# Performance work log

Measured on AMD Instinct MI355X. Metric: run time of the kernel, lower is better.

Reference implementation:

```python
import jax, jax.numpy as jnp
import numpy as np
import math

D_MODEL = 1152
D_K = 1152
NUM_HEADS = 8
HEAD_DIM = D_K // NUM_HEADS  # 144
SIGMA = 2.0
EPS = 1e-6


def rope_2d(keys, positions):
    # keys: [B, N, D]; positions: [B, N, 2] float (x, y)
    B, N, D = keys.shape
    half = D // 2
    quarter = D // 4
    idx = jnp.arange(quarter, dtype=keys.dtype)
    theta = 1.0 / (10000.0 ** (2.0 * idx / half))  # [quarter]
    fx = positions[..., 0][..., None] * theta  # [B, N, quarter]
    fy = positions[..., 1][..., None] * theta

    def apply_rope(part, f):
        p = part.reshape(B, N, quarter, 2)
        c, s = jnp.cos(f), jnp.sin(f)
        o1 = p[..., 0] * c - p[..., 1] * s
        o2 = p[..., 0] * s + p[..., 1] * c
        return jnp.stack([o1, o2], axis=-1).reshape(B, N, half)

    return jnp.concatenate(
        [apply_rope(keys[..., :half], fx), apply_rope(keys[..., half:], fy)], axis=-1
    )


def layernorm_nobias(x, w, eps=EPS):
    mu = jnp.mean(x, axis=-1, keepdims=True)
    var = jnp.mean(jnp.square(x - mu), axis=-1, keepdims=True)
    return (x - mu) * jax.lax.rsqrt(var + eps) * w


def setup_inputs() -> dict:
    key = jax.random.key(0)
    ks = jax.random.split(key, 9)
    T, HW, M = 64, 729, 512
    features = jax.random.normal(ks[0], (T, HW, D_MODEL), dtype=jnp.float32)
    tracks = jax.random.uniform(ks[1], (T, M, 2), dtype=jnp.float32) * 27.0
    track_tokens = jax.random.normal(ks[2], (T, M, D_MODEL), dtype=jnp.float32)
    feature_positions = jax.random.uniform(ks[3], (HW, 2), dtype=jnp.float32) * 27.0
    sc = 1.0 / math.sqrt(D_MODEL)
    # weights stored [in, out]; torch Linear computes x @ W.T with W [out, in]
    W_q = jax.random.normal(ks[4], (D_MODEL, D_K), dtype=jnp.float32) * sc
    W_k = jax.random.normal(ks[5], (D_MODEL, D_K), dtype=jnp.float32) * sc
    q_norm_w = jnp.ones((D_K,), dtype=jnp.float32)
    k_norm_w = jnp.ones((D_K,), dtype=jnp.float32)
    out_proj_w = jax.random.normal(ks[6], (D_MODEL, D_MODEL), dtype=jnp.float32) * sc
    return {
        "features": features,
        "tracks": tracks,
        "track_tokens": track_tokens,
        "feature_positions": feature_positions,
        "W_q": W_q,
        "W_k": W_k,
        "q_norm_w": q_norm_w,
        "k_norm_w": k_norm_w,
        "out_proj_w": out_proj_w,
    }


def reference(features, tracks, track_tokens, feature_positions,
              W_q, W_k, q_norm_w, k_norm_w, out_proj_w):
    T, HW, _ = features.shape
    M = tracks.shape[1]
    Q = track_tokens @ W_q  # [T, M, d_k]
    K = features @ W_k      # [T, HW, d_k]
    feat_pos = jnp.broadcast_to(feature_positions[None], (T, HW, 2))
    K = rope_2d(K, feat_pos)
    Q = layernorm_nobias(Q, q_norm_w)
    K = layernorm_nobias(K, k_norm_w)
    Qh = Q.reshape(T, M, NUM_HEADS, HEAD_DIM).transpose(0, 2, 1, 3)   # [T,H,M,dh]
    Kh = K.reshape(T, HW, NUM_HEADS, HEAD_DIM).transpose(0, 2, 1, 3)  # [T,H,HW,dh]
    Vh = features.reshape(T, HW, NUM_HEADS, -1).transpose(0, 2, 1, 3) # [T,H,HW,dv]
    scores = jnp.einsum("thmd,thnd->thmn", Qh, Kh) / math.sqrt(HEAD_DIM)
    # Gaussian spatial bias: -||track - feat||^2 / (2 sigma^2), shared across heads
    diff = tracks[:, :, None, :] - feature_positions[None, None, :, :]  # [T,M,HW,2]
    dist2 = jnp.sum(jnp.square(diff), axis=-1)  # [T,M,HW]
    bias = -dist2 / (2.0 * SIGMA ** 2)
    scores = scores + bias[:, None, :, :]
    attn = jax.nn.softmax(scores, axis=-1)
    sampled = jnp.einsum("thmn,thnd->thmd", attn, Vh)  # [T,H,M,dv]
    sampled = sampled.transpose(0, 2, 1, 3).reshape(T, M, -1)
    return sampled @ out_proj_w
```

## Files before the change

### kernel.cpp

```cpp
#include <hip/hip_runtime.h>
#include <hip/hip_bf16.h>
#include <math.h>

typedef float f32x4 __attribute__((ext_vector_type(4)));
typedef __bf16 bf16x8 __attribute__((ext_vector_type(8)));

#define T_N 64
#define HW_N 729
#define M_N 512
#define DM 1152
#define NH 8
#define DH 144
#define MQ 32768
#define MK 46656
#define MK_PAD 46720

#define SZ_FEAT ((size_t)MK_PAD * DM * 2)
#define SZ_Q    ((size_t)MQ * DM * 2)
#define SZ_W    ((size_t)DM * DM * 2)
#define OFF_FEAT ((size_t)0)
#define OFF_KN   (OFF_FEAT + SZ_FEAT)
#define OFF_AQ   (OFF_KN + SZ_FEAT)
#define OFF_QN   (OFF_AQ + SZ_Q)
#define OFF_WT   (OFF_QN + SZ_Q)
#define WS_NEED  (OFF_WT + 3 * SZ_W)

__global__ __launch_bounds__(256) void cvt_bf16(const float* __restrict__ src,
                                                __bf16* __restrict__ dst,
                                                long valid4, long total4) {
    long i = (long)blockIdx.x * 256 + threadIdx.x;
    if (i >= total4) return;
    float4 f = {0.f, 0.f, 0.f, 0.f};
    if (i < valid4) f = ((const float4*)src)[i];
    __bf16 tmp[4] = {(__bf16)f.x, (__bf16)f.y, (__bf16)f.z, (__bf16)f.w};
    *((uint2*)(dst + i * 4)) = *((uint2*)tmp);
}

__global__ __launch_bounds__(256) void transpose_w(const float* __restrict__ W,
                                                   __bf16* __restrict__ Wt) {
    __shared__ float tile[32][33];
    const int k0 = blockIdx.x * 32, n0 = blockIdx.y * 32;
    const int tx = threadIdx.x, ty = threadIdx.y;
    #pragma unroll
    for (int i = 0; i < 32; i += 8)
        tile[ty + i][tx] = W[(long)(k0 + ty + i) * DM + n0 + tx];
    __syncthreads();
    #pragma unroll
    for (int i = 0; i < 32; i += 8)
        Wt[(long)(n0 + ty + i) * DM + k0 + tx] = (__bf16)tile[tx][ty + i];
}

template<bool STORE_BF16>
__global__ __launch_bounds__(256) void gemm_bt(const __bf16* __restrict__ A,
                                               const __bf16* __restrict__ Bt,
                                               void* __restrict__ Cout) {
    __shared__ __align__(16) __bf16 As[128 * 40];
    __shared__ __align__(16) __bf16 Bs[128 * 40];
    const int tid  = threadIdx.x;
    const int wave = tid >> 6, lane = tid & 63;
    const int quad = lane >> 4, l16 = lane & 15;
    const int wr = wave >> 1, wc = wave & 1;
    const long m0 = (long)blockIdx.x * 128;
    const long n0 = (long)blockIdx.y * 128;
    f32x4 acc[4][4] = {};
    for (int kt = 0; kt < 36; ++kt) {
        const int k0 = kt * 32;
        __syncthreads();
        #pragma unroll
        for (int s = 0; s < 2; ++s) {
            const int c = s * 256 + tid;
            const int row = c >> 2, kc = c & 3;
            uint4 va = *(const uint4*)(A  + (m0 + row) * DM + k0 + kc * 8);
            uint4 vb = *(const uint4*)(Bt + (n0 + row) * DM + k0 + kc * 8);
            *(uint4*)(As + row * 40 + kc * 8) = va;
            *(uint4*)(Bs + row * 40 + kc * 8) = vb;
        }
        __syncthreads();
        bf16x8 af[4], bfr[4];
        #pragma unroll
        for (int i = 0; i < 4; ++i)
            af[i] = *(const bf16x8*)(As + (wr * 64 + i * 16 + l16) * 40 + quad * 8);
        #pragma unroll
        for (int j = 0; j < 4; ++j)
            bfr[j] = *(const bf16x8*)(Bs + (wc * 64 + j * 16 + l16) * 40 + quad * 8);
        #pragma unroll
        for (int i = 0; i < 4; ++i)
            #pragma unroll
            for (int j = 0; j < 4; ++j)
                acc[i][j] = __builtin_amdgcn_mfma_f32_16x16x32_bf16(af[i], bfr[j], acc[i][j], 0, 0, 0);
    }
    #pragma unroll
    for (int i = 0; i < 4; ++i) {
        #pragma unroll
        for (int j = 0; j < 4; ++j) {
            #pragma unroll
            for (int r = 0; r < 4; ++r) {
                const long row = m0 + wr * 64 + i * 16 + quad * 4 + r;
                const long col = n0 + wc * 64 + j * 16 + l16;
                if constexpr (STORE_BF16)
                    ((__bf16*)Cout)[row * DM + col] = (__bf16)acc[i][j][r];
                else
                    ((float*)Cout)[row * DM + col] = acc[i][j][r];
            }
        }
    }
}

__global__ __launch_bounds__(256) void ln_q(__bf16* __restrict__ Q, const float* __restrict__ w) {
    const long row = blockIdx.x;
    __bf16* p = Q + row * DM;
    const int tid = threadIdx.x;
    float v[5];
    int nv = 0;
    float s = 0.f, s2 = 0.f;
    for (int i = tid; i < DM; i += 256) {
        float x = (float)p[i];
        v[nv++] = x; s += x; s2 += x * x;
    }
    #pragma unroll
    for (int o = 32; o > 0; o >>= 1) { s += __shfl_down(s, o); s2 += __shfl_down(s2, o); }
    __shared__ float red[8];
    if ((tid & 63) == 0) { red[tid >> 6] = s; red[4 + (tid >> 6)] = s2; }
    __syncthreads();
    const float S  = red[0] + red[1] + red[2] + red[3];
    const float S2 = red[4] + red[5] + red[6] + red[7];
    const float mu  = S * (1.f / DM);
    const float var = S2 * (1.f / DM) - mu * mu;
    const float rstd = rsqrtf(var + 1e-6f);
    nv = 0;
    for (int i = tid; i < DM; i += 256)
        p[i] = (__bf16)((v[nv++] - mu) * rstd * w[i]);
}

__global__ __launch_bounds__(256) void rope_ln_k(__bf16* __restrict__ K,
                                                 const float* __restrict__ fpos,
                                                 const float* __restrict__ w) {
    const long row = blockIdx.x;
    const int hw = (int)(row % HW_N);
    const float px = fpos[hw * 2 + 0];
    const float py = fpos[hw * 2 + 1];
    __bf16* p = K + row * DM;
    __shared__ float buf[DM];
    __shared__ float red[8];
    const int tid = threadIdx.x;
    float s = 0.f, s2 = 0.f;
    for (int pr = tid; pr < 576; pr += 256) {
        const bool isx = pr < 288;
        const int  i   = isx ? pr : pr - 288;
        const int  off = isx ? 2 * i : 576 + 2 * i;
        const float pos = isx ? px : py;
        const float theta = powf(10000.f, -(float)i * (1.f / 288.f));
        float sn, cs;
        sincosf(pos * theta, &sn, &cs);
        const float a = (float)p[off], b = (float)p[off + 1];
        const float o1 = a * cs - b * sn;
        const float o2 = a * sn + b * cs;
        buf[off] = o1; buf[off + 1] = o2;
        s += o1 + o2; s2 += o1 * o1 + o2 * o2;
    }
    #pragma unroll
    for (int o = 32; o > 0; o >>= 1) { s += __shfl_down(s, o); s2 += __shfl_down(s2, o); }
    if ((tid & 63) == 0) { red[tid >> 6] = s; red[4 + (tid >> 6)] = s2; }
    __syncthreads();
    const float S  = red[0] + red[1] + red[2] + red[3];
    const float S2 = red[4] + red[5] + red[6] + red[7];
    const float mu  = S * (1.f / DM);
    const float var = S2 * (1.f / DM) - mu * mu;
    const float rstd = rsqrtf(var + 1e-6f);
    for (int i = tid; i < DM; i += 256)
        p[i] = (__bf16)((buf[i] - mu) * rstd * w[i]);
}

__global__ __launch_bounds__(256) void attn(const __bf16* __restrict__ Qn,
                                            const __bf16* __restrict__ Kn,
                                            const __bf16* __restrict__ Vf,
                                            const float* __restrict__ tracks,
                                            const float* __restrict__ fpos,
                                            __bf16* __restrict__ Out) {
    const int b  = blockIdx.x;
    const int qt = b & 7;
    const int th = b >> 3;
    const int h  = th & 7;
    const int t  = th >> 3;
    __shared__ __align__(16) __bf16 Qs[64 * 168];
    __shared__ __align__(16) __bf16 Ks[32 * 168];
    __shared__ __align__(16) __bf16 Vs[32 * 168];
    __shared__ __align__(16) __bf16 Ps[64 * 40];
    __shared__ float trkx[64], trky[64], fpx[32], fpy[32];
    const int tid = threadIdx.x;
    const int wave = tid >> 6, lane = tid & 63;
    const int quad = lane >> 4, l16 = lane & 15;

    {
        const __bf16* qb = Qn + ((long)t * M_N + qt * 64) * DM + h * DH;
        for (int c = tid; c < 64 * 20; c += 256) {
            const int r = c / 20, cc = c % 20;
            uint4 v = {0u, 0u, 0u, 0u};
            if (cc < 18) v = *(const uint4*)(qb + (long)r * DM + cc * 8);
            *(uint4*)(Qs + r * 168 + cc * 8) = v;
        }
        if (tid < 64) {
            const long qr = (long)t * M_N + qt * 64 + tid;
            trkx[tid] = tracks[qr * 2 + 0];
            trky[tid] = tracks[qr * 2 + 1];
        }
    }

    float mrow[4], lrow[4];
    #pragma unroll
    for (int r = 0; r < 4; ++r) { mrow[r] = -1e30f; lrow[r] = 0.f; }
    f32x4 Ot[9] = {};

    for (int kt = 0; kt < 23; ++kt) {
        const int kv0 = kt * 32;
        __syncthreads();
        {
            const __bf16* kb = Kn + ((long)t * HW_N + kv0) * DM + h * DH;
            const __bf16* vb = Vf + ((long)t * HW_N + kv0) * DM + h * DH;
            for (int c = tid; c < 32 * 20; c += 256) {
                const int r = c / 20, cc = c % 20;
                uint4 vk = {0u,0u,0u,0u}, vv = {0u,0u,0u,0u};
                if (cc < 18) {
                    vk = *(const uint4*)(kb + (long)r * DM + cc * 8);
                    vv = *(const uint4*)(vb + (long)r * DM + cc * 8);
                }
                *(uint4*)(Ks + r * 168 + cc * 8) = vk;
                *(uint4*)(Vs + r * 168 + cc * 8) = vv;
            }
            if (tid < 32) {
                const int hw = kv0 + tid;
                if (hw < HW_N) { fpx[tid] = fpos[hw * 2]; fpy[tid] = fpos[hw * 2 + 1]; }
                else           { fpx[tid] = 0.f;          fpy[tid] = 0.f; }
            }
        }
        __syncthreads();
        f32x4 sc[2] = {};
        #pragma unroll
        for (int kc = 0; kc < 5; ++kc) {
            const bf16x8 aq = *(const bf16x8*)(Qs + (wave * 16 + l16) * 168 + kc * 32 + quad * 8);
            #pragma unroll
            for (int j = 0; j < 2; ++j) {
                const bf16x8 bk = *(const bf16x8*)(Ks + (j * 16 + l16) * 168 + kc * 32 + quad * 8);
                sc[j] = __builtin_amdgcn_mfma_f32_16x16x32_bf16(aq, bk, sc[j], 0, 0, 0);
            }
        }
        float fx[2], fy[2]; bool msk[2];
        #pragma unroll
        for (int j = 0; j < 2; ++j) {
            const int cl = j * 16 + l16;
            fx[j] = fpx[cl]; fy[j] = fpy[cl];
            msk[j] = (kv0 + cl) >= HW_N;
        }
        float pvals[4][2];
        float alpha[4];
        #pragma unroll
        for (int r = 0; r < 4; ++r) {
            const int brow = wave * 16 + quad * 4 + r;
            const float tx = trkx[brow], ty = trky[brow];
            float mx = -1e30f;
            #pragma unroll
            for (int j = 0; j < 2; ++j) {
                const float dx = tx - fx[j], dy = ty - fy[j];
                float sv = sc[j][r] * (1.f / 12.f) - (dx * dx + dy * dy) * 0.125f;
                if (msk[j]) sv = -1e30f;
                pvals[r][j] = sv;
                mx = fmaxf(mx, sv);
            }
            #pragma unroll
            for (int o = 1; o < 16; o <<= 1) mx = fmaxf(mx, __shfl_xor(mx, o));
            const float mn = fmaxf(mrow[r], mx);
            alpha[r] = __expf(mrow[r] - mn);
            float rs = 0.f;
            #pragma unroll
            for (int j = 0; j < 2; ++j) {
                const float pv = __expf(pvals[r][j] - mn);
                pvals[r][j] = pv; rs += pv;
            }
            #pragma unroll
            for (int o = 1; o < 16; o <<= 1) rs += __shfl_xor(rs, o);
            lrow[r] = lrow[r] * alpha[r] + rs;
            mrow[r] = mn;
        }
        #pragma unroll
        for (int d = 0; d < 9; ++d)
            #pragma unroll
            for (int r = 0; r < 4; ++r)
                Ot[d][r] *= alpha[r];
        #pragma unroll
        for (int r = 0; r < 4; ++r)
            #pragma unroll
            for (int j = 0; j < 2; ++j)
                Ps[(wave * 16 + quad * 4 + r) * 40 + j * 16 + l16] = (__bf16)pvals[r][j];
        __syncthreads();
        const bf16x8 ap = *(const bf16x8*)(Ps + (wave * 16 + l16) * 40 + quad * 8);
        #pragma unroll
        for (int d = 0; d < 9; ++d) {
            bf16x8 bv;
            #pragma unroll
            for (int jj = 0; jj < 8; ++jj)
                bv[jj] = Vs[(quad * 8 + jj) * 168 + d * 16 + l16];
            Ot[d] = __builtin_amdgcn_mfma_f32_16x16x32_bf16(ap, bv, Ot[d], 0, 0, 0);
        }
    }
    #pragma unroll
    for (int d = 0; d < 9; ++d) {
        #pragma unroll
        for (int r = 0; r < 4; ++r) {
            const long row = (long)t * M_N + qt * 64 + wave * 16 + quad * 4 + r;
            Out[row * DM + h * DH + d * 16 + l16] = (__bf16)(Ot[d][r] / lrow[r]);
        }
    }
}

extern "C" void kernel_launch(void* const* d_in, const int* in_sizes, int n_in,
                              void* d_out, int out_size, void* d_ws, size_t ws_size,
                              hipStream_t stream) {
    const float* features   = (const float*)d_in[0];
    const float* tracks     = (const float*)d_in[1];
    const float* tok        = (const float*)d_in[2];
    const float* fpos       = (const float*)d_in[3];
    const float* W_q        = (const float*)d_in[4];
    const float* W_k        = (const float*)d_in[5];
    const float* q_w        = (const float*)d_in[6];
    const float* k_w        = (const float*)d_in[7];
    const float* W_o        = (const float*)d_in[8];

    if (ws_size < WS_NEED) return;

    char* ws = (char*)d_ws;
    __bf16* feat_bf = (__bf16*)(ws + OFF_FEAT);
    __bf16* kn      = (__bf16*)(ws + OFF_KN);
    __bf16* tok_bf  = (__bf16*)(ws + OFF_AQ);
    __bf16* qn      = (__bf16*)(ws + OFF_QN);
    __bf16* wt_q    = (__bf16*)(ws + OFF_WT);
    __bf16* wt_k    = (__bf16*)(ws + OFF_WT + SZ_W);
    __bf16* wt_o    = (__bf16*)(ws + OFF_WT + 2 * SZ_W);

    {
        const long valid4 = (long)MK * DM / 4, total4 = (long)MK_PAD * DM / 4;
        cvt_bf16<<<(int)((total4 + 255) / 256), 256, 0, stream>>>(features, feat_bf, valid4, total4);
    }
    {
        const long n4 = (long)MQ * DM / 4;
        cvt_bf16<<<(int)((n4 + 255) / 256), 256, 0, stream>>>(tok, tok_bf, n4, n4);
    }
    dim3 tb(32, 8);
    transpose_w<<<dim3(36, 36), tb, 0, stream>>>(W_q, wt_q);
    transpose_w<<<dim3(36, 36), tb, 0, stream>>>(W_k, wt_k);
    transpose_w<<<dim3(36, 36), tb, 0, stream>>>(W_o, wt_o);

    gemm_bt<true><<<dim3(MQ / 128, DM / 128), 256, 0, stream>>>(tok_bf, wt_q, qn);
    gemm_bt<true><<<dim3(MK_PAD / 128, DM / 128), 256, 0, stream>>>(feat_bf, wt_k, kn);

    ln_q<<<MQ, 256, 0, stream>>>(qn, q_w);
    rope_ln_k<<<MK, 256, 0, stream>>>(kn, fpos, k_w);

    __bf16* sampled = tok_bf;
    attn<<<T_N * NH * (M_N / 64), 256, 0, stream>>>(qn, kn, feat_bf, tracks, fpos, sampled);

    gemm_bt<false><<<dim3(MQ / 128, DM / 128), 256, 0, stream>>>(sampled, wt_o, d_out);
}
```

Before: 1.819 ms.

## Rework attention tiling with pre-transposed V and async LDS loads in GEMM

Attention now handles 128 queries per block with 64-key tiles, reads Q and K fragments directly from global memory instead of staging them in LDS, and loads V from a new pre-transposed bf16 layout so the PV MFMA operands become contiguous vector loads rather than scalar gathers. The GEMM switches to global_load_lds async copies with an XOR-swizzled unpadded LDS layout to avoid bank conflicts. A new transpose_v kernel costs an extra pass over features, and the workspace is reorganised so feat_bf and vt share one region. The rope theta is computed with exp2f instead of powf.

New measurement: 1.739 ms. 4.4% less time.

```diff
diff --git a/kernel.cpp b/kernel.cpp
--- a/kernel.cpp
+++ b/kernel.cpp
@@ -7,6 +7,7 @@
 
 #define T_N 64
 #define HW_N 729
+#define HW_P 736
 #define M_N 512
 #define DM 1152
 #define NH 8
@@ -16,14 +17,22 @@
 #define MK_PAD 46720
 
 #define SZ_FEAT ((size_t)MK_PAD * DM * 2)
+#define SZ_VT   ((size_t)T_N * NH * DH * HW_P * 2)
+#define SZ_OV   (SZ_VT > SZ_FEAT ? SZ_VT : SZ_FEAT)
 #define SZ_Q    ((size_t)MQ * DM * 2)
 #define SZ_W    ((size_t)DM * DM * 2)
-#define OFF_FEAT ((size_t)0)
-#define OFF_KN   (OFF_FEAT + SZ_FEAT)
-#define OFF_AQ   (OFF_KN + SZ_FEAT)
-#define OFF_QN   (OFF_AQ + SZ_Q)
-#define OFF_WT   (OFF_QN + SZ_Q)
+#define OFF_KN   ((size_t)0)
+#define OFF_TOK  (OFF_KN + SZ_FEAT)
+#define OFF_QN   (OFF_TOK + SZ_Q)
+#define OFF_OV   (OFF_QN + SZ_Q)
+#define OFF_WT   (OFF_OV + SZ_OV)
 #define WS_NEED  (OFF_WT + 3 * SZ_W)
+
+__device__ __forceinline__ void async_copy16(void* lds, const void* g) {
+    __builtin_amdgcn_global_load_lds(
+        (const __attribute__((address_space(1))) void*)g,
+        (__attribute__((address_space(3))) void*)lds, 16, 0, 0);
+}
 
 __global__ __launch_bounds__(256) void cvt_bf16(const float* __restrict__ src,
                                                 __bf16* __restrict__ dst,
@@ -50,18 +59,42 @@
         Wt[(long)(n0 + ty + i) * DM + k0 + tx] = (__bf16)tile[tx][ty + i];
 }
 
+__global__ __launch_bounds__(256) void transpose_v(const float* __restrict__ f,
+                                                   __bf16* __restrict__ vt) {
+    __shared__ float tile[32][149];
+    const int hw0 = blockIdx.x * 32, h = blockIdx.y, t = blockIdx.z;
+    const int tid = threadIdx.x;
+    for (int c = tid; c < 32 * 36; c += 256) {
+        const int r = c / 36, s = c % 36;
+        const int hw = hw0 + r;
+        float4 v = {0.f, 0.f, 0.f, 0.f};
+        if (hw < HW_N) v = *(const float4*)(f + ((long)t * HW_N + hw) * DM + h * DH + s * 4);
+        tile[r][s * 4 + 0] = v.x; tile[r][s * 4 + 1] = v.y;
+        tile[r][s * 4 + 2] = v.z; tile[r][s * 4 + 3] = v.w;
+    }
+    __syncthreads();
+    for (int c = tid; c < DH * 4; c += 256) {
+        const int d = c >> 2, s = c & 3;
+        __bf16 tmp[8];
+        #pragma unroll
+        for (int i = 0; i < 8; ++i) tmp[i] = (__bf16)tile[s * 8 + i][d];
+        *(uint4*)(vt + ((long)(t * NH + h) * DH + d) * HW_P + hw0 + s * 8) = *(uint4*)tmp;
+    }
+}
+
 template<bool STORE_BF16>
 __global__ __launch_bounds__(256) void gemm_bt(const __bf16* __restrict__ A,
                                                const __bf16* __restrict__ Bt,
                                                void* __restrict__ Cout) {
-    __shared__ __align__(16) __bf16 As[128 * 40];
-    __shared__ __align__(16) __bf16 Bs[128 * 40];
+    __shared__ __align__(16) __bf16 As[128 * 32];
+    __shared__ __align__(16) __bf16 Bs[128 * 32];
     const int tid  = threadIdx.x;
     const int wave = tid >> 6, lane = tid & 63;
     const int quad = lane >> 4, l16 = lane & 15;
     const int wr = wave >> 1, wc = wave & 1;
     const long m0 = (long)blockIdx.x * 128;
     const long n0 = (long)blockIdx.y * 128;
+    const int swzr = quad ^ ((l16 >> 1) & 3);
     f32x4 acc[4][4] = {};
     for (int kt = 0; kt < 36; ++kt) {
         const int k0 = kt * 32;
@@ -69,20 +102,19 @@
         #pragma unroll
         for (int s = 0; s < 2; ++s) {
             const int c = s * 256 + tid;
-            const int row = c >> 2, kc = c & 3;
-            uint4 va = *(const uint4*)(A  + (m0 + row) * DM + k0 + kc * 8);
-            uint4 vb = *(const uint4*)(Bt + (n0 + row) * DM + k0 + kc * 8);
-            *(uint4*)(As + row * 40 + kc * 8) = va;
-            *(uint4*)(Bs + row * 40 + kc * 8) = vb;
+            const int row = c >> 2;
+            const int gkc = (c & 3) ^ ((c >> 3) & 3);
+            async_copy16(As + c * 8, A  + (m0 + row) * DM + k0 + gkc * 8);
+            async_copy16(Bs + c * 8, Bt + (n0 + row) * DM + k0 + gkc * 8);
         }
         __syncthreads();
         bf16x8 af[4], bfr[4];
         #pragma unroll
         for (int i = 0; i < 4; ++i)
-            af[i] = *(const bf16x8*)(As + (wr * 64 + i * 16 + l16) * 40 + quad * 8);
+            af[i] = *(const bf16x8*)(As + (wr * 64 + i * 16 + l16) * 32 + swzr * 8);
         #pragma unroll
         for (int j = 0; j < 4; ++j)
-            bfr[j] = *(const bf16x8*)(Bs + (wc * 64 + j * 16 + l16) * 40 + quad * 8);
+            bfr[j] = *(const bf16x8*)(Bs + (wc * 64 + j * 16 + l16) * 32 + swzr * 8);
         #pragma unroll
         for (int i = 0; i < 4; ++i)
             #pragma unroll
@@ -149,7 +181,7 @@
         const int  i   = isx ? pr : pr - 288;
         const int  off = isx ? 2 * i : 576 + 2 * i;
         const float pos = isx ? px : py;
-        const float theta = powf(10000.f, -(float)i * (1.f / 288.f));
+        const float theta = exp2f((float)i * -0.046137890206768924f);
         float sn, cs;
         sincosf(pos * theta, &sn, &cs);
         const float a = (float)p[off], b = (float)p[off + 1];
@@ -171,143 +203,144 @@
         p[i] = (__bf16)((buf[i] - mu) * rstd * w[i]);
 }
 
-__global__ __launch_bounds__(256) void attn(const __bf16* __restrict__ Qn,
-                                            const __bf16* __restrict__ Kn,
-                                            const __bf16* __restrict__ Vf,
-                                            const float* __restrict__ tracks,
-                                            const float* __restrict__ fpos,
-                                            __bf16* __restrict__ Out) {
+__global__ __launch_bounds__(256, 3) void attn(const __bf16* __restrict__ Qn,
+                                               const __bf16* __restrict__ Kn,
+                                               const __bf16* __restrict__ Vt,
+                                               const float* __restrict__ tracks,
+                                               const float* __restrict__ fpos,
+                                               __bf16* __restrict__ Out) {
+    __shared__ __align__(16) __bf16 VtL[DH * 72];
+    __shared__ __align__(16) __bf16 Ps[128 * 72];
+    __shared__ float2 trkL[128];
     const int b  = blockIdx.x;
-    const int qt = b & 7;
-    const int th = b >> 3;
+    const int qt = b & 3;
+    const int th = b >> 2;
     const int h  = th & 7;
     const int t  = th >> 3;
-    __shared__ __align__(16) __bf16 Qs[64 * 168];
-    __shared__ __align__(16) __bf16 Ks[32 * 168];
-    __shared__ __align__(16) __bf16 Vs[32 * 168];
-    __shared__ __align__(16) __bf16 Ps[64 * 40];
-    __shared__ float trkx[64], trky[64], fpx[32], fpy[32];
     const int tid = threadIdx.x;
     const int wave = tid >> 6, lane = tid & 63;
     const int quad = lane >> 4, l16 = lane & 15;
-
-    {
-        const __bf16* qb = Qn + ((long)t * M_N + qt * 64) * DM + h * DH;
-        for (int c = tid; c < 64 * 20; c += 256) {
-            const int r = c / 20, cc = c % 20;
-            uint4 v = {0u, 0u, 0u, 0u};
-            if (cc < 18) v = *(const uint4*)(qb + (long)r * DM + cc * 8);
-            *(uint4*)(Qs + r * 168 + cc * 8) = v;
-        }
-        if (tid < 64) {
-            const long qr = (long)t * M_N + qt * 64 + tid;
-            trkx[tid] = tracks[qr * 2 + 0];
-            trky[tid] = tracks[qr * 2 + 1];
-        }
-    }
-
-    float mrow[4], lrow[4];
-    #pragma unroll
-    for (int r = 0; r < 4; ++r) { mrow[r] = -1e30f; lrow[r] = 0.f; }
-    f32x4 Ot[9] = {};
-
-    for (int kt = 0; kt < 23; ++kt) {
-        const int kv0 = kt * 32;
-        __syncthreads();
-        {
-            const __bf16* kb = Kn + ((long)t * HW_N + kv0) * DM + h * DH;
-            const __bf16* vb = Vf + ((long)t * HW_N + kv0) * DM + h * DH;
-            for (int c = tid; c < 32 * 20; c += 256) {
-                const int r = c / 20, cc = c % 20;
-                uint4 vk = {0u,0u,0u,0u}, vv = {0u,0u,0u,0u};
-                if (cc < 18) {
-                    vk = *(const uint4*)(kb + (long)r * DM + cc * 8);
-                    vv = *(const uint4*)(vb + (long)r * DM + cc * 8);
+    const int wq = wave * 32;
+
+    if (tid < 128) trkL[tid] = ((const float2*)tracks)[(long)t * M_N + qt * 128 + tid];
+
+    const __bf16* qb = Qn + ((long)t * M_N + qt * 128 + wq) * DM + h * DH;
+    const __bf16* kb = Kn + (long)t * HW_N * DM + h * DH;
+    const __bf16* vb = Vt + (long)(t * NH + h) * DH * HW_P;
+    const __bf16* zpg = Kn + (size_t)MK * DM;
+
+    f32x4 Ot[2][9] = {};
+    float mrow[2][4], lrow[2][4];
+    #pragma unroll
+    for (int rt = 0; rt < 2; ++rt)
+        #pragma unroll
+        for (int r = 0; r < 4; ++r) { mrow[rt][r] = -1e30f; lrow[rt][r] = 0.f; }
+
+    for (int kt = 0; kt < 12; ++kt) {
+        const int kv0 = kt * 64;
+        __syncthreads();
+        for (int c = tid; c < DH * 9; c += 256) {
+            const int r = c / 9, s = c % 9;
+            const __bf16* g = (s < 8 && (kv0 + s * 8 + 8) <= HW_P)
+                                ? vb + (long)r * HW_P + kv0 + s * 8 : zpg;
+            async_copy16(VtL + c * 8, g);
+        }
+        __syncthreads();
+        f32x4 sc[2][4] = {};
+        #pragma unroll
+        for (int kc = 0; kc < 5; ++kc) {
+            bf16x8 aq[2];
+            #pragma unroll
+            for (int rt = 0; rt < 2; ++rt) {
+                uint4 u = {0u, 0u, 0u, 0u};
+                if (kc < 4 || quad < 2)
+                    u = *(const uint4*)(qb + (long)(rt * 16 + l16) * DM + kc * 32 + quad * 8);
+                aq[rt] = *(bf16x8*)&u;
+            }
+            #pragma unroll
+            for (int jt = 0; jt < 4; ++jt) {
+                const bf16x8 bk = *(const bf16x8*)(kb + (long)(kv0 + jt * 16 + l16) * DM + kc * 32 + quad * 8);
+                #pragma unroll
+                for (int rt = 0; rt < 2; ++rt)
+                    sc[rt][jt] = __builtin_amdgcn_mfma_f32_16x16x32_bf16(aq[rt], bk, sc[rt][jt], 0, 0, 0);
+            }
+        }
+        float fx[4], fy[4]; bool msk[4];
+        #pragma unroll
+        for (int jt = 0; jt < 4; ++jt) {
+            const int kv = kv0 + jt * 16 + l16;
+            msk[jt] = kv >= HW_N;
+            float2 fp = {0.f, 0.f};
+            if (!msk[jt]) fp = ((const float2*)fpos)[kv];
+            fx[jt] = fp.x; fy[jt] = fp.y;
+        }
+        float alpha[2][4];
+        #pragma unroll
+        for (int rt = 0; rt < 2; ++rt) {
+            #pragma unroll
+            for (int r = 0; r < 4; ++r) {
+                const int row = wq + rt * 16 + quad * 4 + r;
+                const float tx = trkL[row].x, ty = trkL[row].y;
+                float sv[4];
+                float mx = -1e30f;
+                #pragma unroll
+                for (int jt = 0; jt < 4; ++jt) {
+                    const float dx = tx - fx[jt], dy = ty - fy[jt];
+                    float v = sc[rt][jt][r] * (1.f / 12.f) - (dx * dx + dy * dy) * 0.125f;
+                    if (msk[jt]) v = -1e30f;
+                    sv[jt] = v;
+                    mx = fmaxf(mx, v);
                 }
-                *(uint4*)(Ks + r * 168 + cc * 8) = vk;
-                *(uint4*)(Vs + r * 168 + cc * 8) = vv;
-            }
-            if (tid < 32) {
-                const int hw = kv0 + tid;
-                if (hw < HW_N) { fpx[tid] = fpos[hw * 2]; fpy[tid] = fpos[hw * 2 + 1]; }
-                else           { fpx[tid] = 0.f;          fpy[tid] = 0.f; }
-            }
-        }
-        __syncthreads();
-        f32x4 sc[2] = {};
-        #pragma unroll
-        for (int kc = 0; kc < 5; ++kc) {
-            const bf16x8 aq = *(const bf16x8*)(Qs + (wave * 16 + l16) * 168 + kc * 32 + quad * 8);
-            #pragma unroll
-            for (int j = 0; j < 2; ++j) {
-                const bf16x8 bk = *(const bf16x8*)(Ks + (j * 16 + l16) * 168 + kc * 32 + quad * 8);
-                sc[j] = __builtin_amdgcn_mfma_f32_16x16x32_bf16(aq, bk, sc[j], 0, 0, 0);
-            }
-        }
-        float fx[2], fy[2]; bool msk[2];
-        #pragma unroll
-        for (int j = 0; j < 2; ++j) {
-            const int cl = j * 16 + l16;
-            fx[j] = fpx[cl]; fy[j] = fpy[cl];
-            msk[j] = (kv0 + cl) >= HW_N;
-        }
-        float pvals[4][2];
-        float alpha[4];
+                #pragma unroll
+                for (int o = 1; o < 16; o <<= 1) mx = fmaxf(mx, __shfl_xor(mx, o));
+                const float mn = fmaxf(mrow[rt][r], mx);
+                const float al = __expf(mrow[rt][r] - mn);
+                float rs = 0.f;
+                #pragma unroll
+                for (int jt = 0; jt < 4; ++jt) {
+                    const float p = __expf(sv[jt] - mn);
+                    rs += p;
+                    Ps[row * 72 + jt * 16 + l16] = (__bf16)p;
+                }
+                #pragma unroll
+                for (int o = 1; o < 16; o <<= 1) rs += __shfl_xor(rs, o);
+                lrow[rt][r] = lrow[rt][r] * al + rs;
+                mrow[rt][r] = mn;
+                alpha[rt][r] = al;
+            }
+        }
+        #pragma unroll
+        for (int rt = 0; rt < 2; ++rt)
+            #pragma unroll
+            for (int d = 0; d < 9; ++d)
+                #pragma unroll
+                for (int r = 0; r < 4; ++r)
+                    Ot[rt][d][r] *= alpha[rt][r];
+        __syncthreads();
+        #pragma unroll
+        for (int kh = 0; kh < 2; ++kh) {
+            bf16x8 ap[2];
+            #pragma unroll
+            for (int rt = 0; rt < 2; ++rt)
+                ap[rt] = *(const bf16x8*)(Ps + (wq + rt * 16 + l16) * 72 + kh * 32 + quad * 8);
+            #pragma unroll
+            for (int d = 0; d < 9; ++d) {
+                const bf16x8 bv = *(const bf16x8*)(VtL + (d * 16 + l16) * 72 + kh * 32 + quad * 8);
+                #pragma unroll
+                for (int rt = 0; rt < 2; ++rt)
+                    Ot[rt][d] = __builtin_amdgcn_mfma_f32_16x16x32_bf16(ap[rt], bv, Ot[rt][d], 0, 0, 0);
+            }
+        }
+    }
+    #pragma unroll
+    for (int rt = 0; rt < 2; ++rt) {
         #pragma unroll
         for (int r = 0; r < 4; ++r) {
-            const int brow = wave * 16 + quad * 4 + r;
-            const float tx = trkx[brow], ty = trky[brow];
-            float mx = -1e30f;
-            #pragma unroll
-            for (int j = 0; j < 2; ++j) {
-                const float dx = tx - fx[j], dy = ty - fy[j];
-                float sv = sc[j][r] * (1.f / 12.f) - (dx * dx + dy * dy) * 0.125f;
-                if (msk[j]) sv = -1e30f;
-                pvals[r][j] = sv;
-                mx = fmaxf(mx, sv);
-            }
-            #pragma unroll
-            for (int o = 1; o < 16; o <<= 1) mx = fmaxf(mx, __shfl_xor(mx, o));
-            const float mn = fmaxf(mrow[r], mx);
-            alpha[r] = __expf(mrow[r] - mn);
-            float rs = 0.f;
-            #pragma unroll
-            for (int j = 0; j < 2; ++j) {
-                const float pv = __expf(pvals[r][j] - mn);
-                pvals[r][j] = pv; rs += pv;
-            }
-            #pragma unroll
-            for (int o = 1; o < 16; o <<= 1) rs += __shfl_xor(rs, o);
-            lrow[r] = lrow[r] * alpha[r] + rs;
-            mrow[r] = mn;
-        }
-        #pragma unroll
-        for (int d = 0; d < 9; ++d)
-            #pragma unroll
-            for (int r = 0; r < 4; ++r)
-                Ot[d][r] *= alpha[r];
-        #pragma unroll
-        for (int r = 0; r < 4; ++r)
-            #pragma unroll
-            for (int j = 0; j < 2; ++j)
-                Ps[(wave * 16 + quad * 4 + r) * 40 + j * 16 + l16] = (__bf16)pvals[r][j];
-        __syncthreads();
-        const bf16x8 ap = *(const bf16x8*)(Ps + (wave * 16 + l16) * 40 + quad * 8);
-        #pragma unroll
-        for (int d = 0; d < 9; ++d) {
-            bf16x8 bv;
-            #pragma unroll
-            for (int jj = 0; jj < 8; ++jj)
-                bv[jj] = Vs[(quad * 8 + jj) * 168 + d * 16 + l16];
-            Ot[d] = __builtin_amdgcn_mfma_f32_16x16x32_bf16(ap, bv, Ot[d], 0, 0, 0);
-        }
-    }
-    #pragma unroll
-    for (int d = 0; d < 9; ++d) {
-        #pragma unroll
-        for (int r = 0; r < 4; ++r) {
-            const long row = (long)t * M_N + qt * 64 + wave * 16 + quad * 4 + r;
-            Out[row * DM + h * DH + d * 16 + l16] = (__bf16)(Ot[d][r] / lrow[r]);
+            const float inv = 1.f / lrow[rt][r];
+            const long row = (long)t * M_N + qt * 128 + wq + rt * 16 + quad * 4 + r;
+            #pragma unroll
+            for (int d = 0; d < 9; ++d)
+                Out[row * DM + h * DH + d * 16 + l16] = (__bf16)(Ot[rt][d][r] * inv);
         }
     }
 }
@@ -315,23 +348,24 @@
 extern "C" void kernel_launch(void* const* d_in, const int* in_sizes, int n_in,
                               void* d_out, int out_size, void* d_ws, size_t ws_size,
                               hipStream_t stream) {
-    const float* features   = (const float*)d_in[0];
-    const float* tracks     = (const float*)d_in[1];
-    const float* tok        = (const float*)d_in[2];
-    const float* fpos       = (const float*)d_in[3];
-    const float* W_q        = (const float*)d_in[4];
-    const float* W_k        = (const float*)d_in[5];
-    const float* q_w        = (const float*)d_in[6];
-    const float* k_w        = (const float*)d_in[7];
-    const float* W_o        = (const float*)d_in[8];
+    const float* features = (const float*)d_in[0];
+    const float* tracks   = (const float*)d_in[1];
+    const float* tok      = (const float*)d_in[2];
+    const float* fpos     = (const float*)d_in[3];
+    const float* W_q      = (const float*)d_in[4];
+    const float* W_k      = (const float*)d_in[5];
+    const float* q_w      = (const float*)d_in[6];
+    const float* k_w      = (const float*)d_in[7];
+    const float* W_o      = (const float*)d_in[8];
 
     if (ws_size < WS_NEED) return;
 
     char* ws = (char*)d_ws;
-    __bf16* feat_bf = (__bf16*)(ws + OFF_FEAT);
     __bf16* kn      = (__bf16*)(ws + OFF_KN);
-    __bf16* tok_bf  = (__bf16*)(ws + OFF_AQ);
+    __bf16* tok_bf  = (__bf16*)(ws + OFF_TOK);
     __bf16* qn      = (__bf16*)(ws + OFF_QN);
+    __bf16* feat_bf = (__bf16*)(ws + OFF_OV);
+    __bf16* vt      = (__bf16*)(ws + OFF_OV);
     __bf16* wt_q    = (__bf16*)(ws + OFF_WT);
     __bf16* wt_k    = (__bf16*)(ws + OFF_WT + SZ_W);
     __bf16* wt_o    = (__bf16*)(ws + OFF_WT + 2 * SZ_W);
@@ -355,8 +389,10 @@
     ln_q<<<MQ, 256, 0, stream>>>(qn, q_w);
     rope_ln_k<<<MK, 256, 0, stream>>>(kn, fpos, k_w);
 
+    transpose_v<<<dim3(23, NH, T_N), 256, 0, stream>>>(features, vt);
+
     __bf16* sampled = tok_bf;
-    attn<<<T_N * NH * (M_N / 64), 256, 0, stream>>>(qn, kn, feat_bf, tracks, fpos, sampled);
+    attn<<<T_N * NH * (M_N / 128), 256, 0, stream>>>(qn, kn, vt, tracks, fpos, sampled);
 
     gemm_bt<false><<<dim3(MQ / 128, DM / 128), 256, 0, stream>>>(sampled, wt_o, d_out);
 }
```
